# Kernel optimization log

Measured on AMD Instinct MI355X. Metric: run time of the kernel, lower is better.

## Reference

```python
import jax, jax.numpy as jnp
import numpy as np

L = 2          # num_layers
D = 2048       # embed_dim
HQ = 16        # num_q_heads
HK = 4         # num_kv_heads
HD = D // HQ   # head_size = 128
G = HQ // HK   # q_to_kv_ratio = 4
P = 8192       # embed_dim_proj
V = 32000      # vocab_size
B = 1
S = 2048
EPS = 1e-5
THETA = 500000.0
NEG = -1e30


def setup_inputs() -> dict:
    key = jax.random.key(0)
    ks = jax.random.split(key, 8)
    s = 0.02
    return {
        "tokens": jax.random.randint(ks[0], (B, S), 0, V, dtype=jnp.int32),
        "embed": jax.random.normal(ks[1], (V, D), jnp.float32) * s,
        "attn_norm_w": jnp.ones((L, D), jnp.float32),
        "qkv_w": jax.random.normal(ks[2], (L, D, D + 2 * HK * HD), jnp.float32) * s,
        "attn_out_w": jax.random.normal(ks[3], (L, D, D), jnp.float32) * s,
        "mlp_norm_w": jnp.ones((L, D), jnp.float32),
        "mlp_in_w": jax.random.normal(ks[4], (L, D, 2 * P), jnp.float32) * s,
        "mlp_out_w": jax.random.normal(ks[5], (L, P, D), jnp.float32) * s,
        "final_norm_w": jnp.ones((D,), jnp.float32),
        "lm_head_w": jax.random.normal(ks[6], (D, V), jnp.float32) * s,
    }


def _rms(x, w):
    return w * (x * jax.lax.rsqrt(jnp.mean(x * x, axis=-1, keepdims=True) + EPS))


def _rope_cos_sin():
    inv = 1.0 / (THETA ** (jnp.arange(0, HD, 2, dtype=jnp.float32) / HD))  # [HD/2]
    ang = jnp.arange(S, dtype=jnp.float32)[:, None] * inv[None, :]         # [S, HD/2]
    return jnp.cos(ang), jnp.sin(ang)


def _rope(t, cos, sin):
    # t: [B,S,H,HD]; interleaved complex rotation on (even, odd) pairs
    x = t.reshape(t.shape[:-1] + (HD // 2, 2))
    x0, x1 = x[..., 0], x[..., 1]
    c = cos[None, :, None, :]
    sn = sin[None, :, None, :]
    out = jnp.stack([x0 * c - x1 * sn, x0 * sn + x1 * c], axis=-1)
    return out.reshape(t.shape)


def _layer(x, nw1, wqkv, wo, nw2, wi, wmo, cos, sin, mask):
    # attention block (pre-norm, residual)
    h = _rms(x, nw1)
    qkv = h @ wqkv
    q = qkv[..., :D].reshape(B, S, HQ, HD)
    k = qkv[..., D:D + HK * HD].reshape(B, S, HK, HD)
    v = qkv[..., D + HK * HD:].reshape(B, S, HK, HD)
    q = _rope(q, cos, sin)
    k = _rope(k, cos, sin)
    # GQA: repeat_interleave along head dim
    k = jnp.repeat(k, G, axis=2)
    v = jnp.repeat(v, G, axis=2)
    scores = jnp.einsum('bqhd,bkhd->bhqk', q, k) / np.float32(np.sqrt(HD))
    scores = jnp.where(mask, scores, NEG)
    attn = jax.nn.softmax(scores, axis=-1)
    o = jnp.einsum('bhqk,bkhd->bqhd', attn, v).reshape(B, S, D)
    x = x + o @ wo
    # SwiGLU block (pre-norm, residual)
    h = _rms(x, nw2)
    gu = h @ wi
    gate, up = gu[..., :P], gu[..., P:]
    x = x + (jax.nn.silu(gate) * up) @ wmo
    return x


def reference(tokens, embed, attn_norm_w, qkv_w, attn_out_w, mlp_norm_w,
              mlp_in_w, mlp_out_w, final_norm_w, lm_head_w):
    cos, sin = _rope_cos_sin()
    mask = jnp.tril(jnp.ones((S, S), dtype=bool))  # offset=0 prefill -> causal
    x = embed[tokens]  # [B,S,D]
    for i in range(L):
        x = _layer(x, attn_norm_w[i], qkv_w[i], attn_out_w[i],
                   mlp_norm_w[i], mlp_in_w[i], mlp_out_w[i], cos, sin, mask)
    return _rms(x, final_norm_w) @ lm_head_w  # [B,S,V]
```

## Files before the change

### kernel.cpp

```cpp
#include <hip/hip_runtime.h>
#include <math.h>

#define S_LEN 2048
#define DMODEL 2048
#define NHQ 16
#define NHK 4
#define HDIM 128
#define PDIM 8192
#define VOCAB 32000
#define NQKV 3072
#define EPSI 1e-5f

typedef unsigned short u16;
typedef unsigned int u32;
typedef __bf16 bf16x8 __attribute__((ext_vector_type(8)));
typedef float f32x4 __attribute__((ext_vector_type(4)));

__device__ __forceinline__ u16 f2bf(float f){
  u32 u = __builtin_bit_cast(u32, f);
  u += 0x7fffu + ((u >> 16) & 1u);
  return (u16)(u >> 16);
}
__device__ __forceinline__ float bf2f(u16 h){
  u32 u = ((u32)h) << 16;
  return __builtin_bit_cast(float, u);
}
__device__ __forceinline__ bf16x8 ld8(const u16* p){
  return __builtin_bit_cast(bf16x8, *(const uint4*)p);
}
__device__ __forceinline__ f32x4 mfma16(bf16x8 a, bf16x8 b, f32x4 c){
  return __builtin_amdgcn_mfma_f32_16x16x32_bf16(a, b, c, 0, 0, 0);
}

#define GLOAD_LDS16(gp, lp) __builtin_amdgcn_global_load_lds( \
    (__attribute__((address_space(1))) void*)(gp), \
    (__attribute__((address_space(3))) void*)(lp), 16, 0, 0)

__device__ __forceinline__ bf16x8 lds_frag(const u16* Lb, int R, int g){
  const int Rp = R >> 1;
  const int s8 = (((R & 1) << 2) | g) ^ (Rp & 7);
  return ld8(Lb + Rp * 64 + s8 * 8);
}
__device__ __forceinline__ void stage_sw(const u16* base, long row0, int kstride, int kt,
                                         int q, u16* Ldst_waveuniform){
  const int Rp = q >> 3;
  const int u = (q & 7) ^ (Rp & 7);
  const int R = (Rp << 1) | (u >> 2);
  const u16* gp = base + (row0 + R) * (long)kstride + kt + ((u & 3) << 3);
  GLOAD_LDS16(gp, Ldst_waveuniform);
}

__device__ __forceinline__ void map_bmn(int id0, int nwg, int nbn, int G,
                                        int& bm, int& bn){
  const int cpx = nwg >> 3;
  const int id = (id0 & 7) * cpx + (id0 >> 3);
  const int bmi = id % G;
  const int r2 = id / G;
  bn = r2 % nbn;
  bm = (r2 / nbn) * G + bmi;
}

__global__ void k_embed(const int* __restrict__ tok, const float* __restrict__ emb,
                        float* __restrict__ x){
  const int s = blockIdx.x, t = threadIdx.x;
  const long r = tok[s];
  const float4* src = (const float4*)(emb + r * DMODEL);
  float4* dst = (float4*)(x + (long)s * DMODEL);
  dst[t] = src[t];
  dst[t + 256] = src[t + 256];
}

__global__ void k_rmsnorm(const float* __restrict__ x, const float* __restrict__ w,
                          u16* __restrict__ out){
  const int s = blockIdx.x, t = threadIdx.x;
  const float4* xr = (const float4*)(x + (long)s * DMODEL);
  const float4 a = xr[t], b = xr[t + 256];
  float ss = a.x*a.x + a.y*a.y + a.z*a.z + a.w*a.w
           + b.x*b.x + b.y*b.y + b.z*b.z + b.w*b.w;
  #pragma unroll
  for (int off = 32; off > 0; off >>= 1) ss += __shfl_down(ss, off, 64);
  __shared__ float part[4];
  if ((t & 63) == 0) part[t >> 6] = ss;
  __syncthreads();
  const float r = rsqrtf((part[0] + part[1] + part[2] + part[3]) * (1.f / 2048.f) + EPSI);
  const float4* wr = (const float4*)w;
  const float4 wa = wr[t], wb = wr[t + 256];
  uint2 ua, ub;
  ua.x = (u32)f2bf(a.x*r*wa.x) | ((u32)f2bf(a.y*r*wa.y) << 16);
  ua.y = (u32)f2bf(a.z*r*wa.z) | ((u32)f2bf(a.w*r*wa.w) << 16);
  ub.x = (u32)f2bf(b.x*r*wb.x) | ((u32)f2bf(b.y*r*wb.y) << 16);
  ub.y = (u32)f2bf(b.z*r*wb.z) | ((u32)f2bf(b.w*r*wb.w) << 16);
  *(uint2*)(out + (long)s * DMODEL + 4 * t) = ua;
  *(uint2*)(out + (long)s * DMODEL + 1024 + 4 * t) = ub;
}

__global__ __launch_bounds__(256) void k_convT(const float* __restrict__ W,
                                               u16* __restrict__ Wt, int N, int K){
  const int n0 = blockIdx.x * 64, k0 = blockIdx.y * 64;
  const int t = threadIdx.x;
  __shared__ u16 T[64][72];
  const int r = t >> 4, c = (t & 15) << 2;
  #pragma unroll
  for (int p = 0; p < 4; ++p){
    const int k = p * 16 + r;
    const float4 v = *(const float4*)(W + (long)(k0 + k) * N + n0 + c);
    T[c + 0][k] = f2bf(v.x);
    T[c + 1][k] = f2bf(v.y);
    T[c + 2][k] = f2bf(v.z);
    T[c + 3][k] = f2bf(v.w);
  }
  __syncthreads();
  const int nr = t >> 3, kc = (t & 7) << 3;
  #pragma unroll
  for (int p = 0; p < 2; ++p){
    const int n = p * 32 + nr;
    *(uint4*)(Wt + (long)(n0 + n) * K + k0 + kc) = *(const uint4*)(&T[n][kc]);
  }
}

__global__ __launch_bounds__(256) void k_transV(const u16* __restrict__ qkv,
                                                u16* __restrict__ vT){
  const int s0 = blockIdx.x * 64, d0 = blockIdx.y * 64, kh = blockIdx.z;
  const int t = threadIdx.x;
  __shared__ u16 T[64][72];
  #pragma unroll
  for (int p = 0; p < 4; ++p){
    const int s = p * 16 + (t >> 4);
    const int c = (t & 15) * 4;
    const uint2 v = *(const uint2*)(qkv + (long)(s0 + s) * NQKV + DMODEL + 512 + kh * HDIM + d0 + c);
    T[c + 0][s] = (u16)(v.x);
    T[c + 1][s] = (u16)(v.x >> 16);
    T[c + 2][s] = (u16)(v.y);
    T[c + 3][s] = (u16)(v.y >> 16);
  }
  __syncthreads();
  #pragma unroll
  for (int p = 0; p < 2; ++p){
    const int d = p * 32 + (t >> 3);
    *(uint4*)(vT + ((long)kh * HDIM + d0 + d) * S_LEN + s0 + (t & 7) * 8) =
        *(const uint4*)(&T[d][(t & 7) * 8]);
  }
}

template<int OUT_BF16, int RES>
__global__ __launch_bounds__(256) void k_gemm(const u16* __restrict__ A, const u16* __restrict__ Bt,
                                              void* C, const float* Rs,
                                              int M, int N, int K, int nbn, int G){
  int bm, bn;
  map_bmn(blockIdx.x, gridDim.x, nbn, G, bm, bn);
  const int t = threadIdx.x;
  const int w = t >> 6, lane = t & 63, l15 = lane & 15, g = lane >> 4;
  const int wr = w >> 1, wc = w & 1;
  __shared__ u16 As[4096];
  __shared__ u16 Bs[4096];
  f32x4 acc[4][4] = {};
  const long arow = (long)bm * 128;
  const long brow = (long)bn * 128;
  for (int kt = 0; kt < K; kt += 32){
    __syncthreads();
    #pragma unroll
    for (int c = 0; c < 2; ++c){
      const int q0 = ((w << 1) | c) << 6;
      const int q  = q0 | lane;
      stage_sw(A,  arow, K, kt, q, As + q0 * 8);
      stage_sw(Bt, brow, K, kt, q, Bs + q0 * 8);
    }
    __syncthreads();
    bf16x8 af[4], bfr[4];
    #pragma unroll
    for (int i = 0; i < 4; ++i)
      af[i] = lds_frag(As, wr * 64 + i * 16 + l15, g);
    #pragma unroll
    for (int i = 0; i < 4; ++i)
      bfr[i] = lds_frag(Bs, wc * 64 + i * 16 + l15, g);
    #pragma unroll
    for (int mi = 0; mi < 4; ++mi)
      #pragma unroll
      for (int ni = 0; ni < 4; ++ni)
        acc[mi][ni] = mfma16(af[mi], bfr[ni], acc[mi][ni]);
  }
  const int row0 = bm * 128 + wr * 64, col0 = bn * 128 + wc * 64;
  #pragma unroll
  for (int mi = 0; mi < 4; ++mi){
    #pragma unroll
    for (int ni = 0; ni < 4; ++ni){
      #pragma unroll
      for (int r = 0; r < 4; ++r){
        const long ri = row0 + mi * 16 + g * 4 + r;
        const long ci = col0 + ni * 16 + l15;
        float v = acc[mi][ni][r];
        if (RES) v += Rs[ri * N + ci];
        if (OUT_BF16) ((u16*)C)[ri * N + ci] = f2bf(v);
        else          ((float*)C)[ri * N + ci] = v;
      }
    }
  }
}

__global__ __launch_bounds__(256) void k_gemmsk(const u16* __restrict__ A,
                                                const u16* __restrict__ Bt,
                                                float* __restrict__ P,
                                                int M, int N, int K, int nbn, int G){
  const int ks = blockIdx.y;
  const int KH = K >> 1;
  A  += (long)ks * KH;
  Bt += (long)ks * KH;
  P  += (long)ks * M * N;
  int bm, bn;
  map_bmn(blockIdx.x, gridDim.x, nbn, G, bm, bn);
  const int t = threadIdx.x;
  const int w = t >> 6, lane = t & 63, l15 = lane & 15, g = lane >> 4;
  const int wr = w >> 1, wc = w & 1;
  __shared__ u16 As[4096];
  __shared__ u16 Bs[4096];
  f32x4 acc[4][4] = {};
  const long arow = (long)bm * 128;
  const long brow = (long)bn * 128;
  for (int kt = 0; kt < KH; kt += 32){
    __syncthreads();
    #pragma unroll
    for (int c = 0; c < 2; ++c){
      const int q0 = ((w << 1) | c) << 6;
      const int q  = q0 | lane;
      stage_sw(A,  arow, K, kt, q, As + q0 * 8);
      stage_sw(Bt, brow, K, kt, q, Bs + q0 * 8);
    }
    __syncthreads();
    bf16x8 af[4], bfr[4];
    #pragma unroll
    for (int i = 0; i < 4; ++i)
      af[i] = lds_frag(As, wr * 64 + i * 16 + l15, g);
    #pragma unroll
    for (int i = 0; i < 4; ++i)
      bfr[i] = lds_frag(Bs, wc * 64 + i * 16 + l15, g);
    #pragma unroll
    for (int mi = 0; mi < 4; ++mi)
      #pragma unroll
      for (int ni = 0; ni < 4; ++ni)
        acc[mi][ni] = mfma16(af[mi], bfr[ni], acc[mi][ni]);
  }
  const int row0 = bm * 128 + wr * 64, col0 = bn * 128 + wc * 64;
  #pragma unroll
  for (int mi = 0; mi < 4; ++mi){
    #pragma unroll
    for (int ni = 0; ni < 4; ++ni){
      #pragma unroll
      for (int r = 0; r < 4; ++r){
        const long ri = row0 + mi * 16 + g * 4 + r;
        const long ci = col0 + ni * 16 + l15;
        P[ri * N + ci] = acc[mi][ni][r];
      }
    }
  }
}

__global__ void k_red2(float* __restrict__ x, const float* __restrict__ p0,
                       const float* __restrict__ p1){
  const long i = ((long)blockIdx.x * 256 + threadIdx.x) * 4;
  const float4 a = *(const float4*)(p0 + i);
  const float4 b = *(const float4*)(p1 + i);
  float4 c = *(const float4*)(x + i);
  c.x += a.x + b.x; c.y += a.y + b.y; c.z += a.z + b.z; c.w += a.w + b.w;
  *(float4*)(x + i) = c;
}

template<int OUT_BF16>
__global__ __launch_bounds__(1024, 4) void k_gemmX(const u16* __restrict__ A,
                                                   const u16* __restrict__ Bt,
                                                   void* C, int M, int N, int K){
  __shared__ u16 L[65536];
  const int t = threadIdx.x;
  const int w = t >> 6, lane = t & 63, l15 = lane & 15, g = lane >> 4;
  const int wr = w >> 2, wc = w & 3;
  const int nbm = M >> 8;
  int id = blockIdx.x;
  {
    const int cpx = gridDim.x >> 3;
    id = (id & 7) * cpx + (id >> 3);
  }
  const int bm = id % nbm, bn = id / nbm;
  const int NT = K >> 5;

  const int Rp0 = t >> 3;
  const int u0  = (t & 7) ^ (Rp0 & 7);
  const int R0  = (Rp0 << 1) | (u0 >> 2);
  const int kc0 = (u0 & 3) << 3;
  const u16* pA = A  + ((long)bm * 256 + R0) * (long)K + kc0;
  const u16* pB = Bt + ((long)bn * 256 + R0) * (long)K + kc0;
  const int w0 = (t & ~63) * 8;

  auto stage = [&](int s){
    u16* d = L + s * 16384;
    GLOAD_LDS16(pA, d + w0);
    GLOAD_LDS16(pB, d + 8192 + w0);
    pA += 32; pB += 32;
  };

  stage(0); stage(1); stage(2);
  asm volatile("s_waitcnt vmcnt(4)" ::: "memory");
  __builtin_amdgcn_s_barrier();

  f32x4 acc[4][4] = {};
  for (int tt = 0; tt < NT; ++tt){
    const int slot = tt & 3;
    const u16* sA = L + slot * 16384;
    const u16* sB = sA + 8192;
    bf16x8 af[4], bfr[4];
    #pragma unroll
    for (int mi = 0; mi < 4; ++mi)
      af[mi] = lds_frag(sA, wr * 64 + mi * 16 + l15, g);
    #pragma unroll
    for (int ni = 0; ni < 4; ++ni)
      bfr[ni] = lds_frag(sB, wc * 64 + ni * 16 + l15, g);
    if (tt + 3 < NT) stage((tt + 3) & 3);
    asm volatile("s_waitcnt lgkmcnt(0)" ::: "memory");
    if (tt + 3 < NT)      asm volatile("s_waitcnt vmcnt(4)" ::: "memory");
    else if (tt + 2 < NT) asm volatile("s_waitcnt vmcnt(2)" ::: "memory");
    else if (tt + 1 < NT) asm volatile("s_waitcnt vmcnt(0)" ::: "memory");
    __builtin_amdgcn_s_barrier();
    __builtin_amdgcn_s_setprio(1);
    #pragma unroll
    for (int mi = 0; mi < 4; ++mi)
      #pragma unroll
      for (int ni = 0; ni < 4; ++ni)
        acc[mi][ni] = mfma16(af[mi], bfr[ni], acc[mi][ni]);
    __builtin_amdgcn_s_setprio(0);
  }
  const int row0 = bm * 256 + wr * 64, col0 = bn * 256 + wc * 64;
  #pragma unroll
  for (int mi = 0; mi < 4; ++mi){
    #pragma unroll
    for (int ni = 0; ni < 4; ++ni){
      #pragma unroll
      for (int r = 0; r < 4; ++r){
        const long ri = row0 + mi * 16 + g * 4 + r;
        const long ci = col0 + ni * 16 + l15;
        const float v = acc[mi][ni][r];
        if (OUT_BF16) ((u16*)C)[ri * N + ci] = f2bf(v);
        else          ((float*)C)[ri * N + ci] = v;
      }
    }
  }
}

__global__ void k_rope(u16* __restrict__ qkv){
  const int idx = blockIdx.x * 256 + threadIdx.x;
  const int i = idx & 63;
  const int head = (idx >> 6) % 20;
  const int s = idx / (64 * 20);
  const long base = (long)s * NQKV + (head < NHQ ? head * HDIM : DMODEL + (head - NHQ) * HDIM);
  u32* p = (u32*)(qkv + base + 2 * i);
  const u32 v = *p;
  const float x0 = bf2f((u16)(v & 0xffffu)), x1 = bf2f((u16)(v >> 16));
  const float ang = (float)s * exp2f(-0.29580575889569023f * (float)i);
  float sn, cs;
  sincosf(ang, &sn, &cs);
  const float y0 = x0 * cs - x1 * sn;
  const float y1 = x0 * sn + x1 * cs;
  *p = (u32)f2bf(y0) | ((u32)f2bf(y1) << 16);
}

__global__ __launch_bounds__(256) void k_attn(const u16* __restrict__ qkv,
                                              const u16* __restrict__ vT,
                                              u16* __restrict__ o){
  const int id = blockIdx.x;
  const int xcd = id & 7, j = id >> 3;
  const int kh = xcd >> 1;
  const int h  = (kh << 2) + ((xcd & 1) << 1) + (j & 1);
  const int qb = 31 - (j >> 1);
  const int t = threadIdx.x, w = t >> 6, lane = t & 63, l15 = lane & 15, g = lane >> 4;
  __shared__ u16 Ks[2][8192];
  __shared__ u16 Vs[2][8192];
  __shared__ u16 Ps[4][16 * 72];
  const int q0 = qb * 64 + w * 16;
  bf16x8 aq[4];
  #pragma unroll
  for (int d0 = 0; d0 < 4; ++d0)
    aq[d0] = ld8(qkv + (long)(q0 + l15) * NQKV + h * HDIM + d0 * 32 + g * 8);
  f32x4 acc_o[8] = {};
  float mst[4], lst[4];
  #pragma unroll
  for (int r = 0; r < 4; ++r){ mst[r] = -1e30f; lst[r] = 0.f; }
  const float scale = 0.08838834764831843f;

  auto stageK = [&](int kt, int b){
    #pragma unroll
    for (int p = 0; p < 4; ++p){
      const int q = p * 256 + t;
      const int r = q >> 4, u = q & 15;
      const u16* gp = qkv + (long)(kt * 64 + r) * NQKV + DMODEL + kh * HDIM + ((u ^ (r & 15)) << 3);
      GLOAD_LDS16(gp, Ks[b] + (p * 256 + (t & ~63)) * 8);
    }
  };
  auto stageV = [&](int kt, int b){
    #pragma unroll
    for (int p = 0; p < 4; ++p){
      const int q = p * 256 + t;
      const int r = q >> 3, u = q & 7;
      const u16* gp = vT + ((long)kh * HDIM + r) * S_LEN + kt * 64 + ((u ^ (r & 7)) << 3);
      GLOAD_LDS16(gp, Vs[b] + (p * 256 + (t & ~63)) * 8);
    }
  };

  const int nkt = qb + 1;
  stageK(0, 0); stageV(0, 0);
  for (int kt = 0; kt < nkt; ++kt){
    const int kv0 = kt << 6;
    __builtin_amdgcn_s_barrier();
    if (kt + 1 < nkt){
      stageK(kt + 1, (kt + 1) & 1);
      stageV(kt + 1, (kt + 1) & 1);
      asm volatile("s_waitcnt vmcnt(8)" ::: "memory");
    } else {
      asm volatile("s_waitcnt vmcnt(0)" ::: "memory");
    }
    __builtin_amdgcn_s_barrier();
    const u16* K_ = Ks[kt & 1];
    const u16* V_ = Vs[kt & 1];
    f32x4 sacc[4] = {};
    #pragma unroll
    for (int d0 = 0; d0 < 4; ++d0){
      #pragma unroll
      for (int j2 = 0; j2 < 4; ++j2){
        const bf16x8 bk = ld8(K_ + (j2 * 16 + l15) * 128 + ((((d0 << 2) | g) ^ l15) << 3));
        sacc[j2] = mfma16(aq[d0], bk, sacc[j2]);
      }
    }
    float p[4][4], scl[4];
    #pragma unroll
    for (int r = 0; r < 4; ++r){
      const int qrow = q0 + g * 4 + r;
      float mx = -1e30f;
      #pragma unroll
      for (int j2 = 0; j2 < 4; ++j2){
        float sv = sacc[j2][r] * scale;
        sv = (kv0 + j2 * 16 + l15 <= qrow) ? sv : -1e30f;
        p[j2][r] = sv;
        mx = fmaxf(mx, sv);
      }
      #pragma unroll
      for (int off = 1; off < 16; off <<= 1) mx = fmaxf(mx, __shfl_xor(mx, off, 64));
      const float mnew = fmaxf(mst[r], mx);
      scl[r] = __expf(mst[r] - mnew);
      float rs = 0.f;
      #pragma unroll
      for (int j2 = 0; j2 < 4; ++j2){ p[j2][r] = __expf(p[j2][r] - mnew); rs += p[j2][r]; }
      #pragma unroll
      for (int off = 1; off < 16; off <<= 1) rs += __shfl_xor(rs, off, 64);
      lst[r] = lst[r] * scl[r] + rs;
      mst[r] = mnew;
    }
    #pragma unroll
    for (int n = 0; n < 8; ++n)
      #pragma unroll
      for (int r = 0; r < 4; ++r)
        acc_o[n][r] *= scl[r];
    #pragma unroll
    for (int j2 = 0; j2 < 4; ++j2)
      #pragma unroll
      for (int r = 0; r < 4; ++r)
        Ps[w][(g * 4 + r) * 72 + j2 * 16 + l15] = f2bf(p[j2][r]);
    #pragma unroll
    for (int kk = 0; kk < 2; ++kk){
      const bf16x8 pa = ld8(Ps[w] + l15 * 72 + kk * 32 + g * 8);
      #pragma unroll
      for (int n = 0; n < 8; ++n){
        const int row = n * 16 + l15;
        const bf16x8 bv = ld8(V_ + row * 64 + ((((kk << 2) | g) ^ (l15 & 7)) << 3));
        acc_o[n] = mfma16(pa, bv, acc_o[n]);
      }
    }
    asm volatile("s_waitcnt lgkmcnt(0)" ::: "memory");
  }
  #pragma unroll
  for (int n = 0; n < 8; ++n){
    #pragma unroll
    for (int r = 0; r < 4; ++r){
      const float ov = acc_o[n][r] / lst[r];
      o[(long)(q0 + g * 4 + r) * DMODEL + h * HDIM + n * 16 + l15] = f2bf(ov);
    }
  }
}

__global__ void k_swiglu(const u16* __restrict__ gu, u16* __restrict__ out){
  const long idx = ((long)blockIdx.x * 256 + threadIdx.x) * 8;
  const long s = idx >> 13;
  const int j = (int)(idx & 8191);
  const u16* gp = gu + s * 16384 + j;
  const uint4 gv = *(const uint4*)gp;
  const uint4 uv = *(const uint4*)(gp + PDIM);
  const u32 gw[4] = {gv.x, gv.y, gv.z, gv.w};
  const u32 uw[4] = {uv.x, uv.y, uv.z, uv.w};
  u32 ow[4];
  #pragma unroll
  for (int k = 0; k < 4; ++k){
    const float g0 = bf2f((u16)(gw[k] & 0xffffu)), g1 = bf2f((u16)(gw[k] >> 16));
    const float u0 = bf2f((u16)(uw[k] & 0xffffu)), u1 = bf2f((u16)(uw[k] >> 16));
    const float s0 = g0 / (1.f + __expf(-g0)) * u0;
    const float s1 = g1 / (1.f + __expf(-g1)) * u1;
    ow[k] = (u32)f2bf(s0) | ((u32)f2bf(s1) << 16);
  }
  uint4 ro; ro.x = ow[0]; ro.y = ow[1]; ro.z = ow[2]; ro.w = ow[3];
  *(uint4*)(out + idx) = ro;
}

extern "C" void kernel_launch(void* const* d_in, const int* in_sizes, int n_in,
                              void* d_out, int out_size, void* d_ws, size_t ws_size,
                              hipStream_t stream){
  const int*   tokens       = (const int*)d_in[0];
  const float* embed        = (const float*)d_in[1];
  const float* attn_norm_w  = (const float*)d_in[2];
  const float* qkv_w        = (const float*)d_in[3];
  const float* attn_out_w   = (const float*)d_in[4];
  const float* mlp_norm_w   = (const float*)d_in[5];
  const float* mlp_in_w     = (const float*)d_in[6];
  const float* mlp_out_w    = (const float*)d_in[7];
  const float* final_norm_w = (const float*)d_in[8];
  const float* lm_head_w    = (const float*)d_in[9];

  char* ws = (char*)d_ws;
  float* xf  = (float*)(ws);
  u16* hbf   = (u16*)(ws + 16777216);
  u16* qkvb  = (u16*)(ws + 25165824);
  u16* obf   = (u16*)(ws + 37748736);
  u16* gub   = (u16*)(ws + 46137344);
  u16* hb2   = (u16*)(ws + 113246208);
  u16* wbuf  = (u16*)(ws + 146800640);
  u16* vTb   = (u16*)(ws + 277872640);
  float* pp  = (float*)gub;

  k_embed<<<S_LEN, 256, 0, stream>>>(tokens, embed, xf);
  for (int l = 0; l < 2; ++l){
    k_rmsnorm<<<S_LEN, 256, 0, stream>>>(xf, attn_norm_w + (long)l * DMODEL, hbf);
    k_convT<<<dim3(NQKV/64, DMODEL/64), 256, 0, stream>>>(
        qkv_w + (long)l * DMODEL * NQKV, wbuf, NQKV, DMODEL);
    k_gemm<1,0><<<(S_LEN/128) * (NQKV/128), 256, 0, stream>>>(
        hbf, wbuf, qkvb, nullptr, S_LEN, NQKV, DMODEL, NQKV/128, 4);
    k_rope<<<(S_LEN * 20 * 64) / 256, 256, 0, stream>>>(qkvb);
    k_transV<<<dim3(S_LEN/64, 2, 4), 256, 0, stream>>>(qkvb, vTb);
    k_attn<<<512, 256, 0, stream>>>(qkvb, vTb, obf);
    k_convT<<<dim3(DMODEL/64, DMODEL/64), 256, 0, stream>>>(
        attn_out_w + (long)l * DMODEL * DMODEL, wbuf, DMODEL, DMODEL);
    k_gemm<0,1><<<(S_LEN/128) * (DMODEL/128), 256, 0, stream>>>(
        obf, wbuf, xf, xf, S_LEN, DMODEL, DMODEL, DMODEL/128, 4);
    k_rmsnorm<<<S_LEN, 256, 0, stream>>>(xf, mlp_norm_w + (long)l * DMODEL, hbf);
    k_convT<<<dim3((2*PDIM)/64, DMODEL/64), 256, 0, stream>>>(
        mlp_in_w + (long)l * DMODEL * 2 * PDIM, wbuf, 2*PDIM, DMODEL);
    k_gemmX<1><<<(S_LEN/256) * ((2*PDIM)/256), 1024, 0, stream>>>(
        hbf, wbuf, gub, S_LEN, 2*PDIM, DMODEL);
    k_swiglu<<<(S_LEN * PDIM / 8) / 256, 256, 0, stream>>>(gub, hb2);
    k_convT<<<dim3(DMODEL/64, PDIM/64), 256, 0, stream>>>(
        mlp_out_w + (long)l * PDIM * DMODEL, wbuf, DMODEL, PDIM);
    k_gemmsk<<<dim3((S_LEN/128) * (DMODEL/128), 2), 256, 0, stream>>>(
        hb2, wbuf, pp, S_LEN, DMODEL, PDIM, DMODEL/128, 2);
    k_red2<<<(S_LEN * DMODEL) / 1024, 256, 0, stream>>>(
        xf, pp, pp + (long)S_LEN * DMODEL);
  }
  k_rmsnorm<<<S_LEN, 256, 0, stream>>>(xf, final_norm_w, hbf);
  k_convT<<<dim3(VOCAB/64, DMODEL/64), 256, 0, stream>>>(lm_head_w, wbuf, VOCAB, DMODEL);
  k_gemmX<0><<<(S_LEN/256) * (VOCAB/256), 1024, 0, stream>>>(
      hbf, wbuf, (float*)d_out, S_LEN, VOCAB, DMODEL);
}
```

Measured before the change: 1.396 ms.

## Fuse SwiGLU into MLP-in GEMM epilogue and restructure attention blocks

Permutes the MLP input weight rows during conversion so every 256-column GEMM tile holds 128 matching gate and up columns. A new GEMM kernel then applies SiLU(gate)*up in its epilogue through LDS and writes bf16 output directly, removing the separate SwiGLU kernel and the round trip of the gate/up intermediate. Attention is also regrouped into 512-thread blocks that serve two query heads sharing one KV head, so each K/V tile is staged once for both heads. The grid no longer uses the XCD-aware, largest-first ordering, which may hurt load balance under causal masking.

```diff
diff --git a/kernel.cpp b/kernel.cpp
--- a/kernel.cpp
+++ b/kernel.cpp
@@ -115,6 +115,33 @@
   for (int p = 0; p < 2; ++p){
     const int n = p * 32 + nr;
     *(uint4*)(Wt + (long)(n0 + n) * K + k0 + kc) = *(const uint4*)(&T[n][kc]);
+  }
+}
+
+__global__ __launch_bounds__(256) void k_convTmi(const float* __restrict__ W,
+                                                 u16* __restrict__ Wt, int N, int K){
+  const int n0 = blockIdx.x * 64, k0 = blockIdx.y * 64;
+  const int t = threadIdx.x;
+  __shared__ u16 T[64][72];
+  const int r = t >> 4, c = (t & 15) << 2;
+  #pragma unroll
+  for (int p = 0; p < 4; ++p){
+    const int k = p * 16 + r;
+    const float4 v = *(const float4*)(W + (long)(k0 + k) * N + n0 + c);
+    T[c + 0][k] = f2bf(v.x);
+    T[c + 1][k] = f2bf(v.y);
+    T[c + 2][k] = f2bf(v.z);
+    T[c + 3][k] = f2bf(v.w);
+  }
+  __syncthreads();
+  int drow0;
+  if (n0 < PDIM) drow0 = (n0 >> 7) * 256 + (n0 & 127);
+  else { const int m0 = n0 - PDIM; drow0 = (m0 >> 7) * 256 + 128 + (m0 & 127); }
+  const int nr = t >> 3, kc = (t & 7) << 3;
+  #pragma unroll
+  for (int p = 0; p < 2; ++p){
+    const int n = p * 32 + nr;
+    *(uint4*)(Wt + (long)(drow0 + n) * K + k0 + kc) = *(const uint4*)(&T[n][kc]);
   }
 }
 
@@ -343,6 +370,101 @@
   }
 }
 
+__global__ __launch_bounds__(1024, 4) void k_gemmXswi(const u16* __restrict__ A,
+                                                      const u16* __restrict__ Bt,
+                                                      u16* __restrict__ O,
+                                                      int M, int K){
+  __shared__ u16 L[65536];
+  const int t = threadIdx.x;
+  const int w = t >> 6, lane = t & 63, l15 = lane & 15, g = lane >> 4;
+  const int wr = w >> 2, wc = w & 3;
+  const int nbm = M >> 8;
+  int id = blockIdx.x;
+  {
+    const int cpx = gridDim.x >> 3;
+    id = (id & 7) * cpx + (id >> 3);
+  }
+  const int bm = id % nbm, bn = id / nbm;
+  const int NT = K >> 5;
+
+  const int Rp0 = t >> 3;
+  const int u0  = (t & 7) ^ (Rp0 & 7);
+  const int R0  = (Rp0 << 1) | (u0 >> 2);
+  const int kc0 = (u0 & 3) << 3;
+  const u16* pA = A  + ((long)bm * 256 + R0) * (long)K + kc0;
+  const u16* pB = Bt + ((long)bn * 256 + R0) * (long)K + kc0;
+  const int w0 = (t & ~63) * 8;
+
+  auto stage = [&](int s){
+    u16* d = L + s * 16384;
+    GLOAD_LDS16(pA, d + w0);
+    GLOAD_LDS16(pB, d + 8192 + w0);
+    pA += 32; pB += 32;
+  };
+
+  stage(0); stage(1); stage(2);
+  asm volatile("s_waitcnt vmcnt(4)" ::: "memory");
+  __builtin_amdgcn_s_barrier();
+
+  f32x4 acc[4][4] = {};
+  for (int tt = 0; tt < NT; ++tt){
+    const int slot = tt & 3;
+    const u16* sA = L + slot * 16384;
+    const u16* sB = sA + 8192;
+    bf16x8 af[4], bfr[4];
+    #pragma unroll
+    for (int mi = 0; mi < 4; ++mi)
+      af[mi] = lds_frag(sA, wr * 64 + mi * 16 + l15, g);
+    #pragma unroll
+    for (int ni = 0; ni < 4; ++ni)
+      bfr[ni] = lds_frag(sB, wc * 64 + ni * 16 + l15, g);
+    if (tt + 3 < NT) stage((tt + 3) & 3);
+    asm volatile("s_waitcnt lgkmcnt(0)" ::: "memory");
+    if (tt + 3 < NT)      asm volatile("s_waitcnt vmcnt(4)" ::: "memory");
+    else if (tt + 2 < NT) asm volatile("s_waitcnt vmcnt(2)" ::: "memory");
+    else if (tt + 1 < NT) asm volatile("s_waitcnt vmcnt(0)" ::: "memory");
+    __builtin_amdgcn_s_barrier();
+    __builtin_amdgcn_s_setprio(1);
+    #pragma unroll
+    for (int mi = 0; mi < 4; ++mi)
+      #pragma unroll
+      for (int ni = 0; ni < 4; ++ni)
+        acc[mi][ni] = mfma16(af[mi], bfr[ni], acc[mi][ni]);
+    __builtin_amdgcn_s_setprio(0);
+  }
+  __syncthreads();
+  float* U = (float*)L;
+  if (wc >= 2){
+    const int base = ((wr << 1) | (wc - 2)) * 4096;
+    #pragma unroll
+    for (int mi = 0; mi < 4; ++mi)
+      #pragma unroll
+      for (int ni = 0; ni < 4; ++ni)
+        #pragma unroll
+        for (int r = 0; r < 4; ++r)
+          U[base + (mi * 16 + g * 4 + r) * 64 + ni * 16 + l15] = acc[mi][ni][r];
+  }
+  __syncthreads();
+  if (wc < 2){
+    const int base = ((wr << 1) | wc) * 4096;
+    #pragma unroll
+    for (int mi = 0; mi < 4; ++mi){
+      #pragma unroll
+      for (int ni = 0; ni < 4; ++ni){
+        #pragma unroll
+        for (int r = 0; r < 4; ++r){
+          const float gv = acc[mi][ni][r];
+          const float uv = U[base + (mi * 16 + g * 4 + r) * 64 + ni * 16 + l15];
+          const float ov = gv / (1.f + __expf(-gv)) * uv;
+          const long ri = bm * 256 + wr * 64 + mi * 16 + g * 4 + r;
+          const int ci = bn * 128 + wc * 64 + ni * 16 + l15;
+          O[ri * PDIM + ci] = f2bf(ov);
+        }
+      }
+    }
+  }
+}
+
 __global__ void k_rope(u16* __restrict__ qkv){
   const int idx = blockIdx.x * 256 + threadIdx.x;
   const int i = idx & 63;
@@ -360,19 +482,19 @@
   *p = (u32)f2bf(y0) | ((u32)f2bf(y1) << 16);
 }
 
-__global__ __launch_bounds__(256) void k_attn(const u16* __restrict__ qkv,
+__global__ __launch_bounds__(512) void k_attn(const u16* __restrict__ qkv,
                                               const u16* __restrict__ vT,
                                               u16* __restrict__ o){
-  const int id = blockIdx.x;
-  const int xcd = id & 7, j = id >> 3;
-  const int kh = xcd >> 1;
-  const int h  = (kh << 2) + ((xcd & 1) << 1) + (j & 1);
-  const int qb = 31 - (j >> 1);
-  const int t = threadIdx.x, w = t >> 6, lane = t & 63, l15 = lane & 15, g = lane >> 4;
+  const int qb = blockIdx.x;
+  const int kh = blockIdx.y >> 1;
+  const int h  = (kh << 2) + ((blockIdx.y & 1) << 1) + (threadIdx.x >> 8);
+  const int t = threadIdx.x, lane = t & 63, l15 = lane & 15, g = lane >> 4;
+  const int ws = (t >> 6) & 3;
+  const int wv = t >> 6;
   __shared__ u16 Ks[2][8192];
   __shared__ u16 Vs[2][8192];
-  __shared__ u16 Ps[4][16 * 72];
-  const int q0 = qb * 64 + w * 16;
+  __shared__ u16 Ps[8][16 * 72];
+  const int q0 = qb * 64 + ws * 16;
   bf16x8 aq[4];
   #pragma unroll
   for (int d0 = 0; d0 < 4; ++d0)
@@ -385,20 +507,20 @@
 
   auto stageK = [&](int kt, int b){
     #pragma unroll
-    for (int p = 0; p < 4; ++p){
-      const int q = p * 256 + t;
+    for (int p = 0; p < 2; ++p){
+      const int q = p * 512 + t;
       const int r = q >> 4, u = q & 15;
       const u16* gp = qkv + (long)(kt * 64 + r) * NQKV + DMODEL + kh * HDIM + ((u ^ (r & 15)) << 3);
-      GLOAD_LDS16(gp, Ks[b] + (p * 256 + (t & ~63)) * 8);
+      GLOAD_LDS16(gp, Ks[b] + (p * 512 + (t & ~63)) * 8);
     }
   };
   auto stageV = [&](int kt, int b){
     #pragma unroll
-    for (int p = 0; p < 4; ++p){
-      const int q = p * 256 + t;
+    for (int p = 0; p < 2; ++p){
+      const int q = p * 512 + t;
       const int r = q >> 3, u = q & 7;
       const u16* gp = vT + ((long)kh * HDIM + r) * S_LEN + kt * 64 + ((u ^ (r & 7)) << 3);
-      GLOAD_LDS16(gp, Vs[b] + (p * 256 + (t & ~63)) * 8);
+      GLOAD_LDS16(gp, Vs[b] + (p * 512 + (t & ~63)) * 8);
     }
   };
 
@@ -410,7 +532,7 @@
     if (kt + 1 < nkt){
       stageK(kt + 1, (kt + 1) & 1);
       stageV(kt + 1, (kt + 1) & 1);
-      asm volatile("s_waitcnt vmcnt(8)" ::: "memory");
+      asm volatile("s_waitcnt vmcnt(4)" ::: "memory");
     } else {
       asm volatile("s_waitcnt vmcnt(0)" ::: "memory");
     }
@@ -459,10 +581,10 @@
     for (int j2 = 0; j2 < 4; ++j2)
       #pragma unroll
       for (int r = 0; r < 4; ++r)
-        Ps[w][(g * 4 + r) * 72 + j2 * 16 + l15] = f2bf(p[j2][r]);
+        Ps[wv][(g * 4 + r) * 72 + j2 * 16 + l15] = f2bf(p[j2][r]);
     #pragma unroll
     for (int kk = 0; kk < 2; ++kk){
-      const bf16x8 pa = ld8(Ps[w] + l15 * 72 + kk * 32 + g * 8);
+      const bf16x8 pa = ld8(Ps[wv] + l15 * 72 + kk * 32 + g * 8);
       #pragma unroll
       for (int n = 0; n < 8; ++n){
         const int row = n * 16 + l15;
@@ -480,28 +602,6 @@
       o[(long)(q0 + g * 4 + r) * DMODEL + h * HDIM + n * 16 + l15] = f2bf(ov);
     }
   }
-}
-
-__global__ void k_swiglu(const u16* __restrict__ gu, u16* __restrict__ out){
-  const long idx = ((long)blockIdx.x * 256 + threadIdx.x) * 8;
-  const long s = idx >> 13;
-  const int j = (int)(idx & 8191);
-  const u16* gp = gu + s * 16384 + j;
-  const uint4 gv = *(const uint4*)gp;
-  const uint4 uv = *(const uint4*)(gp + PDIM);
-  const u32 gw[4] = {gv.x, gv.y, gv.z, gv.w};
-  const u32 uw[4] = {uv.x, uv.y, uv.z, uv.w};
-  u32 ow[4];
-  #pragma unroll
-  for (int k = 0; k < 4; ++k){
-    const float g0 = bf2f((u16)(gw[k] & 0xffffu)), g1 = bf2f((u16)(gw[k] >> 16));
-    const float u0 = bf2f((u16)(uw[k] & 0xffffu)), u1 = bf2f((u16)(uw[k] >> 16));
-    const float s0 = g0 / (1.f + __expf(-g0)) * u0;
-    const float s1 = g1 / (1.f + __expf(-g1)) * u1;
-    ow[k] = (u32)f2bf(s0) | ((u32)f2bf(s1) << 16);
-  }
-  uint4 ro; ro.x = ow[0]; ro.y = ow[1]; ro.z = ow[2]; ro.w = ow[3];
-  *(uint4*)(out + idx) = ro;
 }
 
 extern "C" void kernel_launch(void* const* d_in, const int* in_sizes, int n_in,
@@ -538,17 +638,16 @@
         hbf, wbuf, qkvb, nullptr, S_LEN, NQKV, DMODEL, NQKV/128, 4);
     k_rope<<<(S_LEN * 20 * 64) / 256, 256, 0, stream>>>(qkvb);
     k_transV<<<dim3(S_LEN/64, 2, 4), 256, 0, stream>>>(qkvb, vTb);
-    k_attn<<<512, 256, 0, stream>>>(qkvb, vTb, obf);
+    k_attn<<<dim3(S_LEN/64, 8), 512, 0, stream>>>(qkvb, vTb, obf);
     k_convT<<<dim3(DMODEL/64, DMODEL/64), 256, 0, stream>>>(
         attn_out_w + (long)l * DMODEL * DMODEL, wbuf, DMODEL, DMODEL);
     k_gemm<0,1><<<(S_LEN/128) * (DMODEL/128), 256, 0, stream>>>(
         obf, wbuf, xf, xf, S_LEN, DMODEL, DMODEL, DMODEL/128, 4);
     k_rmsnorm<<<S_LEN, 256, 0, stream>>>(xf, mlp_norm_w + (long)l * DMODEL, hbf);
-    k_convT<<<dim3((2*PDIM)/64, DMODEL/64), 256, 0, stream>>>(
+    k_convTmi<<<dim3((2*PDIM)/64, DMODEL/64), 256, 0, stream>>>(
         mlp_in_w + (long)l * DMODEL * 2 * PDIM, wbuf, 2*PDIM, DMODEL);
-    k_gemmX<1><<<(S_LEN/256) * ((2*PDIM)/256), 1024, 0, stream>>>(
-        hbf, wbuf, gub, S_LEN, 2*PDIM, DMODEL);
-    k_swiglu<<<(S_LEN * PDIM / 8) / 256, 256, 0, stream>>>(gub, hb2);
+    k_gemmXswi<<<(S_LEN/256) * ((2*PDIM)/256), 1024, 0, stream>>>(
+        hbf, wbuf, hb2, S_LEN, DMODEL);
     k_convT<<<dim3(DMODEL/64, PDIM/64), 256, 0, stream>>>(
         mlp_out_w + (long)l * PDIM * DMODEL, wbuf, DMODEL, PDIM);
     k_gemmsk<<<dim3((S_LEN/128) * (DMODEL/128), 2), 256, 0, stream>>>(
```

After: 1.388 ms. Within noise of the previous version (-0.5%).
